# Optimization experiments

Hardware: AMD Instinct MI355X
Metric: run time of the kernel (lower is better)

Reference implementation:

```python
import jax, jax.numpy as jnp
import numpy as np

B, N, C, H, W = 8, 64, 256, 100, 100
PROJ_C, HID, EMB = 256, 128, 64
GN_EPS = 1e-5
NORM_EPS = 1e-6


def setup_inputs() -> dict:
    key = jax.random.key(0)
    ks = jax.random.split(key, 8)
    features = jax.random.normal(ks[0], (B, C, H, W), dtype=jnp.float32)
    boxes_xyxy = jax.random.uniform(ks[1], (B, N, 4), dtype=jnp.float32)  # normalized boxes in [0,1]
    conv_w = jax.random.normal(ks[2], (PROJ_C, C), dtype=jnp.float32) * (1.0 / np.sqrt(C))  # 1x1 conv, no bias
    gn_w = jnp.ones((PROJ_C,), dtype=jnp.float32)
    gn_b = jnp.zeros((PROJ_C,), dtype=jnp.float32)
    w1 = jax.random.normal(ks[3], (PROJ_C, HID), dtype=jnp.float32) * (1.0 / np.sqrt(PROJ_C))
    b1 = jnp.zeros((HID,), dtype=jnp.float32)
    w2 = jax.random.normal(ks[4], (HID, EMB), dtype=jnp.float32) * (1.0 / np.sqrt(HID))
    b2 = jnp.zeros((EMB,), dtype=jnp.float32)
    return {"features": features, "boxes_xyxy": boxes_xyxy, "conv_w": conv_w,
            "gn_w": gn_w, "gn_b": gn_b, "w1": w1, "b1": b1, "w2": w2, "b2": b2}


def _silu(x):
    return x * jax.nn.sigmoid(x)


def _forward(features, boxes_xyxy, conv_w, gn_w, gn_b, w1, b1, w2, b2):
    # feature_proj: 1x1 conv (no bias) -> GroupNorm(groups=1) -> SiLU
    y = jnp.einsum('bchw,oc->bohw', features, conv_w)
    mu = y.mean(axis=(1, 2, 3), keepdims=True)
    var = y.var(axis=(1, 2, 3), keepdims=True)
    y = (y - mu) * jax.lax.rsqrt(var + GN_EPS)
    y = y * gn_w[None, :, None, None] + gn_b[None, :, None, None]
    src = _silu(y)  # [B,PROJ_C,H,W]

    # project normalized boxes to feature coords (normalized_boxes=True)
    x1 = jnp.minimum(boxes_xyxy[..., 0], boxes_xyxy[..., 2]) * W
    x2 = jnp.maximum(boxes_xyxy[..., 0], boxes_xyxy[..., 2]) * W
    y1 = jnp.minimum(boxes_xyxy[..., 1], boxes_xyxy[..., 3]) * H
    y2 = jnp.maximum(boxes_xyxy[..., 1], boxes_xyxy[..., 3]) * H
    x1 = jnp.clip(jnp.floor(jnp.clip(x1, 0.0, W)), 0.0, W)
    x2 = jnp.clip(jnp.ceil(jnp.clip(x2, 0.0, W)), 0.0, W)
    y1 = jnp.clip(jnp.floor(jnp.clip(y1, 0.0, H)), 0.0, H)
    y2 = jnp.clip(jnp.ceil(jnp.clip(y2, 0.0, H)), 0.0, H)

    # separable region masks: region is rows y1:y2, cols x1:x2
    hs = jnp.arange(H, dtype=jnp.float32)
    ws = jnp.arange(W, dtype=jnp.float32)
    my = ((hs >= y1[..., None]) & (hs < y2[..., None])).astype(src.dtype)  # [B,N,H]
    mx = ((ws >= x1[..., None]) & (ws < x2[..., None])).astype(src.dtype)  # [B,N,W]

    region_sum = jnp.einsum('bnh,bnw,bchw->bnc', my, mx, src)
    count = my.sum(-1) * mx.sum(-1)  # [B,N]
    pooled = jnp.where(count[..., None] > 0, region_sum / jnp.maximum(count[..., None], 1.0), 0.0)

    # embedding MLP + L2 normalize (torch F.normalize semantics)
    raw = _silu(pooled @ w1 + b1) @ w2 + b2
    norm = jnp.linalg.norm(raw, axis=-1, keepdims=True)
    emb = raw / jnp.maximum(norm, NORM_EPS)
    return emb, raw, pooled


def reference(features, boxes_xyxy, conv_w, gn_w, gn_b, w1, b1, w2, b2):
    return _forward(features, boxes_xyxy, conv_w, gn_w, gn_b, w1, b1, w2, b2)
```

## Files before the change

### kernel.cpp

```cpp
#include <hip/hip_runtime.h>
#include <math.h>

#define HWq 10000
#define Cq 256
#define Oq 256

typedef __attribute__((ext_vector_type(8))) short short8v;
typedef __attribute__((ext_vector_type(8))) unsigned short ushort8v;
typedef __attribute__((ext_vector_type(4))) float f32x4;

__device__ __forceinline__ short f2bf(float f) {
    unsigned u = __float_as_uint(f);
    return (short)((u + 0x7FFFu + ((u >> 16) & 1u)) >> 16);
}
__device__ __forceinline__ float bf2f(unsigned short u) {
    return __uint_as_float((unsigned)u << 16);
}

__device__ __forceinline__ int swz(int row, int g) {
    return g ^ (row & 3) ^ ((row >> 2) & 1);
}

__global__ __launch_bounds__(256) void conv_mfma(const float* __restrict__ feat,
                                                 const float* __restrict__ convw,
                                                 unsigned short* __restrict__ y,
                                                 float* __restrict__ stats) {
    __shared__ __align__(16) short Albuf[128 * 32];
    __shared__ __align__(16) short Blbuf[128 * 32];
    __shared__ float redbuf[8];

    const int b  = blockIdx.z;
    const int o0 = blockIdx.y * 128;
    const int p0 = blockIdx.x * 128;
    const int t  = threadIdx.x;
    const int w  = t >> 6;
    const int l  = t & 63;
    const int wo = (w >> 1) * 64;
    const int wp = (w & 1) * 64;

    const float* fb = feat + (size_t)b * Cq * HWq;

    f32x4 acc[4][4];
    #pragma unroll
    for (int i = 0; i < 4; ++i)
        #pragma unroll
        for (int j = 0; j < 4; ++j)
            acc[i][j] = (f32x4){0.f, 0.f, 0.f, 0.f};

    const int oA0 = t >> 2;
    const int oA1 = oA0 + 64;
    const int kuA = t & 3;
    const float* aptr0 = convw + (size_t)(o0 + oA0) * Cq + kuA * 8;
    const float* aptr1 = convw + (size_t)(o0 + oA1) * Cq + kuA * 8;

    int pgB[2];
    #pragma unroll
    for (int pass = 0; pass < 2; ++pass) {
        int pg = p0 + pass * 64 + l;
        pgB[pass] = (pg > HWq - 1) ? (HWq - 1) : pg;
    }

    const int fr_g = l >> 4;
    const int fr_r = l & 15;

    float4 ra0, ra1, ra2, ra3;
    float  rb[2][8];

    auto LOADG = [&](int k0) {
        ra0 = *(const float4*)(aptr0 + k0);
        ra1 = *(const float4*)(aptr0 + k0 + 4);
        ra2 = *(const float4*)(aptr1 + k0);
        ra3 = *(const float4*)(aptr1 + k0 + 4);
        #pragma unroll
        for (int pass = 0; pass < 2; ++pass) {
            const float* fk = fb + (size_t)(k0 + w * 8) * HWq + pgB[pass];
            #pragma unroll
            for (int jj = 0; jj < 8; ++jj)
                rb[pass][jj] = fk[(size_t)jj * HWq];
        }
    };

    LOADG(0);

    for (int k0 = 0; k0 < Cq; k0 += 32) {
        if (k0) __syncthreads();

        {
            short8v s;
            s[0]=f2bf(ra0.x); s[1]=f2bf(ra0.y); s[2]=f2bf(ra0.z); s[3]=f2bf(ra0.w);
            s[4]=f2bf(ra1.x); s[5]=f2bf(ra1.y); s[6]=f2bf(ra1.z); s[7]=f2bf(ra1.w);
            *(short8v*)((char*)Albuf + oA0 * 64 + swz(oA0, kuA) * 16) = s;
            short8v s2;
            s2[0]=f2bf(ra2.x); s2[1]=f2bf(ra2.y); s2[2]=f2bf(ra2.z); s2[3]=f2bf(ra2.w);
            s2[4]=f2bf(ra3.x); s2[5]=f2bf(ra3.y); s2[6]=f2bf(ra3.z); s2[7]=f2bf(ra3.w);
            *(short8v*)((char*)Albuf + oA1 * 64 + swz(oA1, kuA) * 16) = s2;
            #pragma unroll
            for (int pass = 0; pass < 2; ++pass) {
                short8v sb;
                #pragma unroll
                for (int jj = 0; jj < 8; ++jj) sb[jj] = f2bf(rb[pass][jj]);
                int p = pass * 64 + l;
                *(short8v*)((char*)Blbuf + p * 64 + swz(p, w) * 16) = sb;
            }
        }
        __syncthreads();

        if (k0 < Cq - 32) LOADG(k0 + 32);

        short8v af[4], bfv[4];
        #pragma unroll
        for (int i = 0; i < 4; ++i) {
            int row = wo + i * 16 + fr_r;
            af[i] = *(const short8v*)((const char*)Albuf + row * 64 + swz(row, fr_g) * 16);
        }
        #pragma unroll
        for (int j = 0; j < 4; ++j) {
            int row = wp + j * 16 + fr_r;
            bfv[j] = *(const short8v*)((const char*)Blbuf + row * 64 + swz(row, fr_g) * 16);
        }
        #pragma unroll
        for (int i = 0; i < 4; ++i)
            #pragma unroll
            for (int j = 0; j < 4; ++j)
                acc[i][j] = __builtin_amdgcn_mfma_f32_16x16x32_bf16(af[i], bfv[j], acc[i][j], 0, 0, 0);
    }

    float lsum = 0.f, lsq = 0.f;
    #pragma unroll
    for (int i = 0; i < 4; ++i) {
        const int obase = o0 + wo + i * 16 + (l >> 4) * 4;
        #pragma unroll
        for (int j = 0; j < 4; ++j) {
            const int p = p0 + wp + j * 16 + (l & 15);
            if (p < HWq) {
                #pragma unroll
                for (int r = 0; r < 4; ++r) {
                    float v = acc[i][j][r];
                    y[((size_t)(b * Oq + obase + r)) * HWq + p] = (unsigned short)f2bf(v);
                    lsum += v;
                    lsq  += v * v;
                }
            }
        }
    }
    #pragma unroll
    for (int m = 1; m < 64; m <<= 1) {
        lsum += __shfl_xor(lsum, m);
        lsq  += __shfl_xor(lsq, m);
    }
    if (l == 0) { redbuf[w] = lsum; redbuf[4 + w] = lsq; }
    __syncthreads();
    if (t == 0) {
        atomicAdd(&stats[b],     redbuf[0] + redbuf[1] + redbuf[2] + redbuf[3]);
        atomicAdd(&stats[8 + b], redbuf[4] + redbuf[5] + redbuf[6] + redbuf[7]);
    }
}

__global__ __launch_bounds__(256) void integral_pool(const unsigned short* __restrict__ y,
                                                     const float* __restrict__ boxes,
                                                     const float* __restrict__ stats,
                                                     const float* __restrict__ gnw,
                                                     const float* __restrict__ gnb,
                                                     float* __restrict__ pooled) {
    __shared__ float Sl[10000];

    const int plane = blockIdx.x;
    const int b = plane >> 8;
    const int c = plane & 255;
    const int t = threadIdx.x;
    const int wave = t >> 6;
    const int lane = t & 63;

    const float invM = 1.f / 2560000.f;
    const float mu   = stats[b] * invM;
    const float msq  = stats[8 + b] * invM;
    const float rs   = rsqrtf(msq - mu * mu + 1e-5f);
    const float scale = gnw[c] * rs;
    const float shift = gnb[c] - mu * scale;

    const ushort8v* yp8 = (const ushort8v*)(y + (size_t)plane * HWq);

    #pragma unroll
    for (int i = 0; i < 5; ++i) {
        int chunk = t + i * 256;
        if (chunk < 1250) {
            ushort8v u = yp8[chunk];
            float* dst = &Sl[chunk * 8];
            #pragma unroll
            for (int k = 0; k < 8; ++k) {
                float v = bf2f(u[k]) * scale + shift;
                dst[k] = v / (1.f + __expf(-v));
            }
        }
    }
    __syncthreads();

    for (int r = wave; r < 100; r += 4) {
        float* row = &Sl[r * 100];
        float v = row[lane];
        #pragma unroll
        for (int m = 1; m < 64; m <<= 1) {
            float u = __shfl_up(v, m);
            if (lane >= m) v += u;
        }
        row[lane] = v;
        float total = __shfl(v, 63);
        float w2 = (lane < 36) ? row[64 + lane] : 0.f;
        #pragma unroll
        for (int m = 1; m < 64; m <<= 1) {
            float u = __shfl_up(w2, m);
            if (lane >= m) w2 += u;
        }
        w2 += total;
        if (lane < 36) row[64 + lane] = w2;
    }
    __syncthreads();

    {
        const int r0 = wave * 25;
        float accA = 0.f, accB = 0.f;
        const bool hasB = lane < 36;
        const int cA = lane, cB = 64 + lane;
        for (int r = r0; r < r0 + 25; ++r) {
            accA += Sl[r * 100 + cA];
            Sl[r * 100 + cA] = accA;
            if (hasB) {
                accB += Sl[r * 100 + cB];
                Sl[r * 100 + cB] = accB;
            }
        }
    }
    __syncthreads();
    {
        const int cA = lane, cB = 64 + lane;
        const bool hasB = lane < 36;
        float s0A = Sl[24 * 100 + cA], s1A = Sl[49 * 100 + cA], s2A = Sl[74 * 100 + cA];
        float s0B = 0.f, s1B = 0.f, s2B = 0.f;
        if (hasB) { s0B = Sl[24 * 100 + cB]; s1B = Sl[49 * 100 + cB]; s2B = Sl[74 * 100 + cB]; }
        float offA = (wave >= 1 ? s0A : 0.f) + (wave >= 2 ? s1A : 0.f) + (wave >= 3 ? s2A : 0.f);
        float offB = (wave >= 1 ? s0B : 0.f) + (wave >= 2 ? s1B : 0.f) + (wave >= 3 ? s2B : 0.f);
        __syncthreads();
        if (wave >= 1) {
            const int r0 = wave * 25;
            for (int r = r0; r < r0 + 25; ++r) {
                Sl[r * 100 + cA] += offA;
                if (hasB) Sl[r * 100 + cB] += offB;
            }
        }
    }
    __syncthreads();

    {
        const int grp = lane >> 2;
        const int j   = lane & 3;
        const int n   = wave * 16 + grp;
        const float4 bx = *(const float4*)(boxes + ((size_t)b * 64 + n) * 4);

        float x1f = fminf(bx.x, bx.z) * 100.f;
        float x2f = fmaxf(bx.x, bx.z) * 100.f;
        float y1f = fminf(bx.y, bx.w) * 100.f;
        float y2f = fmaxf(bx.y, bx.w) * 100.f;
        x1f = fminf(fmaxf(floorf(fminf(fmaxf(x1f, 0.f), 100.f)), 0.f), 100.f);
        x2f = fminf(fmaxf(ceilf (fminf(fmaxf(x2f, 0.f), 100.f)), 0.f), 100.f);
        y1f = fminf(fmaxf(floorf(fminf(fmaxf(y1f, 0.f), 100.f)), 0.f), 100.f);
        y2f = fminf(fmaxf(ceilf (fminf(fmaxf(y2f, 0.f), 100.f)), 0.f), 100.f);
        const int ix1 = (int)x1f, ix2 = (int)x2f;
        const int iy1 = (int)y1f, iy2 = (int)y2f;
        const int cnt = (ix2 - ix1) * (iy2 - iy1);

        const int hy = (j & 2) ? iy2 - 1 : iy1 - 1;
        const int hx = (j & 1) ? ix2 - 1 : ix1 - 1;
        float v = 0.f;
        if (hy >= 0 && hx >= 0) v = Sl[hy * 100 + hx];
        if (j == 1 || j == 2) v = -v;
        v += __shfl_xor(v, 1);
        v += __shfl_xor(v, 2);
        if (j == 0)
            pooled[((size_t)b * 64 + n) * Cq + c] = (cnt > 0) ? v / (float)cnt : 0.f;
    }
}

__global__ __launch_bounds__(128) void mlp_kernel(const float* __restrict__ pooled,
                                                  const float* __restrict__ w1,
                                                  const float* __restrict__ b1,
                                                  const float* __restrict__ w2,
                                                  const float* __restrict__ b2,
                                                  float* __restrict__ emb,
                                                  float* __restrict__ raw) {
    __shared__ float ps[256];
    __shared__ float hs[128];
    const int bn = blockIdx.x;
    const int t  = threadIdx.x;

    ps[t]       = pooled[(size_t)bn * 256 + t];
    ps[t + 128] = pooled[(size_t)bn * 256 + t + 128];
    __syncthreads();

    float a = b1[t];
    #pragma unroll 8
    for (int c = 0; c < 256; ++c) a += ps[c] * w1[c * 128 + t];
    hs[t] = a / (1.f + __expf(-a));
    __syncthreads();

    if (t < 64) {
        float r = b2[t];
        #pragma unroll 8
        for (int h = 0; h < 128; ++h) r += hs[h] * w2[h * 64 + t];
        raw[(size_t)bn * 64 + t] = r;
        float s = r * r;
        #pragma unroll
        for (int m = 1; m < 64; m <<= 1) s += __shfl_xor(s, m);
        float nrm = fmaxf(sqrtf(s), 1e-6f);
        emb[(size_t)bn * 64 + t] = r / nrm;
    }
}

extern "C" void kernel_launch(void* const* d_in, const int* in_sizes, int n_in,
                              void* d_out, int out_size, void* d_ws, size_t ws_size,
                              hipStream_t stream) {
    const float* feat  = (const float*)d_in[0];
    const float* boxes = (const float*)d_in[1];
    const float* convw = (const float*)d_in[2];
    const float* gnw   = (const float*)d_in[3];
    const float* gnb   = (const float*)d_in[4];
    const float* w1    = (const float*)d_in[5];
    const float* b1    = (const float*)d_in[6];
    const float* w2    = (const float*)d_in[7];
    const float* b2    = (const float*)d_in[8];

    float* out    = (float*)d_out;
    float* emb    = out;
    float* raw    = out + 32768;
    float* pooled = out + 65536;

    unsigned short* y = (unsigned short*)d_ws;
    float* stats = (float*)((char*)d_ws + (size_t)8 * 256 * 10000 * 2);

    hipMemsetAsync(stats, 0, 16 * sizeof(float), stream);

    dim3 g1((HWq + 127) / 128, 2, 8);
    conv_mfma<<<g1, 256, 0, stream>>>(feat, convw, y, stats);

    integral_pool<<<2048, 256, 0, stream>>>(y, boxes, stats, gnw, gnb, pooled);

    mlp_kernel<<<512, 128, 0, stream>>>(pooled, w1, b1, w2, b2, emb, raw);
}
```

Measured before the change: 243.1 us.

## Double-buffer conv LDS tiles and replace 2D integral image with row prefix sums

The conv GEMM now uses two LDS buffers, so the next k-tile is written while MFMAs run on the current one, cutting one barrier per iteration. The pooling kernel drops the full 2D integral image (column scans plus cross-wave fixups and extra barriers). It computes only per-row prefix sums, two pixels per lane with a wave scan, and each box sums row differences over its height with 4 lanes per box. This trades the column-scan passes for a per-box loop over up to 100 rows, which may bring LDS bank conflicts and load imbalance across boxes.

```diff
diff --git a/kernel.cpp b/kernel.cpp
--- a/kernel.cpp
+++ b/kernel.cpp
@@ -6,7 +6,6 @@
 #define Oq 256
 
 typedef __attribute__((ext_vector_type(8))) short short8v;
-typedef __attribute__((ext_vector_type(8))) unsigned short ushort8v;
 typedef __attribute__((ext_vector_type(4))) float f32x4;
 
 __device__ __forceinline__ short f2bf(float f) {
@@ -25,8 +24,8 @@
                                                  const float* __restrict__ convw,
                                                  unsigned short* __restrict__ y,
                                                  float* __restrict__ stats) {
-    __shared__ __align__(16) short Albuf[128 * 32];
-    __shared__ __align__(16) short Blbuf[128 * 32];
+    __shared__ __align__(16) short Al[2][128 * 32];
+    __shared__ __align__(16) short Bl[2][128 * 32];
     __shared__ float redbuf[8];
 
     const int b  = blockIdx.z;
@@ -80,49 +79,54 @@
         }
     };
 
+    auto WRITE = [&](int bi) {
+        short8v s;
+        s[0]=f2bf(ra0.x); s[1]=f2bf(ra0.y); s[2]=f2bf(ra0.z); s[3]=f2bf(ra0.w);
+        s[4]=f2bf(ra1.x); s[5]=f2bf(ra1.y); s[6]=f2bf(ra1.z); s[7]=f2bf(ra1.w);
+        *(short8v*)((char*)Al[bi] + oA0 * 64 + swz(oA0, kuA) * 16) = s;
+        short8v s2;
+        s2[0]=f2bf(ra2.x); s2[1]=f2bf(ra2.y); s2[2]=f2bf(ra2.z); s2[3]=f2bf(ra2.w);
+        s2[4]=f2bf(ra3.x); s2[5]=f2bf(ra3.y); s2[6]=f2bf(ra3.z); s2[7]=f2bf(ra3.w);
+        *(short8v*)((char*)Al[bi] + oA1 * 64 + swz(oA1, kuA) * 16) = s2;
+        #pragma unroll
+        for (int pass = 0; pass < 2; ++pass) {
+            short8v sb;
+            #pragma unroll
+            for (int jj = 0; jj < 8; ++jj) sb[jj] = f2bf(rb[pass][jj]);
+            int p = pass * 64 + l;
+            *(short8v*)((char*)Bl[bi] + p * 64 + swz(p, w) * 16) = sb;
+        }
+    };
+
     LOADG(0);
-
+    WRITE(0);
+    LOADG(32);
+    __syncthreads();
+
+    int cur = 0;
     for (int k0 = 0; k0 < Cq; k0 += 32) {
-        if (k0) __syncthreads();
-
-        {
-            short8v s;
-            s[0]=f2bf(ra0.x); s[1]=f2bf(ra0.y); s[2]=f2bf(ra0.z); s[3]=f2bf(ra0.w);
-            s[4]=f2bf(ra1.x); s[5]=f2bf(ra1.y); s[6]=f2bf(ra1.z); s[7]=f2bf(ra1.w);
-            *(short8v*)((char*)Albuf + oA0 * 64 + swz(oA0, kuA) * 16) = s;
-            short8v s2;
-            s2[0]=f2bf(ra2.x); s2[1]=f2bf(ra2.y); s2[2]=f2bf(ra2.z); s2[3]=f2bf(ra2.w);
-            s2[4]=f2bf(ra3.x); s2[5]=f2bf(ra3.y); s2[6]=f2bf(ra3.z); s2[7]=f2bf(ra3.w);
-            *(short8v*)((char*)Albuf + oA1 * 64 + swz(oA1, kuA) * 16) = s2;
-            #pragma unroll
-            for (int pass = 0; pass < 2; ++pass) {
-                short8v sb;
-                #pragma unroll
-                for (int jj = 0; jj < 8; ++jj) sb[jj] = f2bf(rb[pass][jj]);
-                int p = pass * 64 + l;
-                *(short8v*)((char*)Blbuf + p * 64 + swz(p, w) * 16) = sb;
-            }
-        }
-        __syncthreads();
-
-        if (k0 < Cq - 32) LOADG(k0 + 32);
-
         short8v af[4], bfv[4];
         #pragma unroll
         for (int i = 0; i < 4; ++i) {
             int row = wo + i * 16 + fr_r;
-            af[i] = *(const short8v*)((const char*)Albuf + row * 64 + swz(row, fr_g) * 16);
+            af[i] = *(const short8v*)((const char*)Al[cur] + row * 64 + swz(row, fr_g) * 16);
         }
         #pragma unroll
         for (int j = 0; j < 4; ++j) {
             int row = wp + j * 16 + fr_r;
-            bfv[j] = *(const short8v*)((const char*)Blbuf + row * 64 + swz(row, fr_g) * 16);
+            bfv[j] = *(const short8v*)((const char*)Bl[cur] + row * 64 + swz(row, fr_g) * 16);
+        }
+        if (k0 + 32 < Cq) {
+            WRITE(cur ^ 1);
+            if (k0 + 64 < Cq) LOADG(k0 + 64);
         }
         #pragma unroll
         for (int i = 0; i < 4; ++i)
             #pragma unroll
             for (int j = 0; j < 4; ++j)
                 acc[i][j] = __builtin_amdgcn_mfma_f32_16x16x32_bf16(af[i], bfv[j], acc[i][j], 0, 0, 0);
+        __syncthreads();
+        cur ^= 1;
     }
 
     float lsum = 0.f, lsq = 0.f;
@@ -167,9 +171,8 @@
     const int plane = blockIdx.x;
     const int b = plane >> 8;
     const int c = plane & 255;
-    const int t = threadIdx.x;
-    const int wave = t >> 6;
-    const int lane = t & 63;
+    const int wave = threadIdx.x >> 6;
+    const int lane = threadIdx.x & 63;
 
     const float invM = 1.f / 2560000.f;
     const float mu   = stats[b] * invM;
@@ -178,73 +181,41 @@
     const float scale = gnw[c] * rs;
     const float shift = gnb[c] - mu * scale;
 
-    const ushort8v* yp8 = (const ushort8v*)(y + (size_t)plane * HWq);
-
-    #pragma unroll
-    for (int i = 0; i < 5; ++i) {
-        int chunk = t + i * 256;
-        if (chunk < 1250) {
-            ushort8v u = yp8[chunk];
-            float* dst = &Sl[chunk * 8];
-            #pragma unroll
-            for (int k = 0; k < 8; ++k) {
-                float v = bf2f(u[k]) * scale + shift;
-                dst[k] = v / (1.f + __expf(-v));
+    const unsigned short* yp = y + (size_t)plane * HWq;
+
+    for (int i = 0; i < 25; i += 2) {
+        const int r0 = wave + 4 * i;
+        const int r1 = r0 + 4;
+        const bool has1 = (i + 1) < 25;
+        float a0 = 0.f, b0 = 0.f, a1 = 0.f, b1 = 0.f;
+        if (lane < 50) {
+            ushort2 u0 = *(const ushort2*)(yp + r0 * 100 + 2 * lane);
+            float v0 = bf2f(u0.x) * scale + shift;
+            float v1 = bf2f(u0.y) * scale + shift;
+            a0 = v0 / (1.f + __expf(-v0));
+            b0 = v1 / (1.f + __expf(-v1));
+            if (has1) {
+                ushort2 u1 = *(const ushort2*)(yp + r1 * 100 + 2 * lane);
+                float w0 = bf2f(u1.x) * scale + shift;
+                float w1 = bf2f(u1.y) * scale + shift;
+                a1 = w0 / (1.f + __expf(-w0));
+                b1 = w1 / (1.f + __expf(-w1));
             }
         }
-    }
-    __syncthreads();
-
-    for (int r = wave; r < 100; r += 4) {
-        float* row = &Sl[r * 100];
-        float v = row[lane];
+        float p0 = a0 + b0;
+        float p1 = a1 + b1;
         #pragma unroll
         for (int m = 1; m < 64; m <<= 1) {
-            float u = __shfl_up(v, m);
-            if (lane >= m) v += u;
-        }
-        row[lane] = v;
-        float total = __shfl(v, 63);
-        float w2 = (lane < 36) ? row[64 + lane] : 0.f;
-        #pragma unroll
-        for (int m = 1; m < 64; m <<= 1) {
-            float u = __shfl_up(w2, m);
-            if (lane >= m) w2 += u;
-        }
-        w2 += total;
-        if (lane < 36) row[64 + lane] = w2;
-    }
-    __syncthreads();
-
-    {
-        const int r0 = wave * 25;
-        float accA = 0.f, accB = 0.f;
-        const bool hasB = lane < 36;
-        const int cA = lane, cB = 64 + lane;
-        for (int r = r0; r < r0 + 25; ++r) {
-            accA += Sl[r * 100 + cA];
-            Sl[r * 100 + cA] = accA;
-            if (hasB) {
-                accB += Sl[r * 100 + cB];
-                Sl[r * 100 + cB] = accB;
-            }
-        }
-    }
-    __syncthreads();
-    {
-        const int cA = lane, cB = 64 + lane;
-        const bool hasB = lane < 36;
-        float s0A = Sl[24 * 100 + cA], s1A = Sl[49 * 100 + cA], s2A = Sl[74 * 100 + cA];
-        float s0B = 0.f, s1B = 0.f, s2B = 0.f;
-        if (hasB) { s0B = Sl[24 * 100 + cB]; s1B = Sl[49 * 100 + cB]; s2B = Sl[74 * 100 + cB]; }
-        float offA = (wave >= 1 ? s0A : 0.f) + (wave >= 2 ? s1A : 0.f) + (wave >= 3 ? s2A : 0.f);
-        float offB = (wave >= 1 ? s0B : 0.f) + (wave >= 2 ? s1B : 0.f) + (wave >= 3 ? s2B : 0.f);
-        __syncthreads();
-        if (wave >= 1) {
-            const int r0 = wave * 25;
-            for (int r = r0; r < r0 + 25; ++r) {
-                Sl[r * 100 + cA] += offA;
-                if (hasB) Sl[r * 100 + cB] += offB;
+            float t0 = __shfl_up(p0, m);
+            float t1 = __shfl_up(p1, m);
+            if (lane >= m) { p0 += t0; p1 += t1; }
+        }
+        if (lane < 50) {
+            float2 o0 = {p0 - b0, p0};
+            *(float2*)(&Sl[r0 * 100 + 2 * lane]) = o0;
+            if (has1) {
+                float2 o1 = {p1 - b1, p1};
+                *(float2*)(&Sl[r1 * 100 + 2 * lane]) = o1;
             }
         }
     }
@@ -268,11 +239,16 @@
         const int iy1 = (int)y1f, iy2 = (int)y2f;
         const int cnt = (ix2 - ix1) * (iy2 - iy1);
 
-        const int hy = (j & 2) ? iy2 - 1 : iy1 - 1;
-        const int hx = (j & 1) ? ix2 - 1 : ix1 - 1;
         float v = 0.f;
-        if (hy >= 0 && hx >= 0) v = Sl[hy * 100 + hx];
-        if (j == 1 || j == 2) v = -v;
+        if (cnt > 0) {
+            const int colR = ix2 - 1;
+            const int colL = ix1 - 1;
+            for (int h = iy1 + j; h < iy2; h += 4) {
+                float s = Sl[h * 100 + colR];
+                if (colL >= 0) s -= Sl[h * 100 + colL];
+                v += s;
+            }
+        }
         v += __shfl_xor(v, 1);
         v += __shfl_xor(v, 2);
         if (j == 0)
```

After: 230.3 us. 5.3% less time.
